# Kernel tuning notes

Measured on AMD Instinct MI355X. Metric: run time of the kernel, lower is better.

Reference implementation:

```python
import jax, jax.numpy as jnp
import numpy as np

B, H, W, D, C = 2, 16, 16, 16, 128
UNITS = 128
BN_EPS = 1e-3  # keras BatchNormalization default epsilon


def setup_inputs() -> dict:
    key = jax.random.key(0)
    ks = jax.random.split(key, 12)
    lim = np.sqrt(3.0 / C)  # VarianceScaling(1.0, fan_avg, uniform)
    inp = {
        "x": jax.random.normal(ks[0], (B, H, W, D, C), dtype=jnp.float32),
        "gamma": jnp.ones((C,), jnp.float32),
        "beta": jnp.zeros((C,), jnp.float32),
        "moving_mean": jax.random.normal(ks[1], (C,), jnp.float32) * 0.1,
        "moving_var": jnp.ones((C,), jnp.float32) + 0.1 * jax.random.uniform(ks[2], (C,)),
        "Wq": jax.random.uniform(ks[3], (C, UNITS), jnp.float32, -lim, lim),
        "bq": jnp.zeros((UNITS,), jnp.float32),
        "Wk": jax.random.uniform(ks[4], (C, UNITS), jnp.float32, -lim, lim),
        "bk": jnp.zeros((UNITS,), jnp.float32),
        "Wv": jax.random.uniform(ks[5], (C, UNITS), jnp.float32, -lim, lim),
        "bv": jnp.zeros((UNITS,), jnp.float32),
        # proj uses kernel_init(0.0) -> effectively ~0; use tiny scale to keep grads nonzero
        "Wp": jax.random.uniform(ks[6], (UNITS, UNITS), jnp.float32, -1e-5, 1e-5),
        "bp": jnp.zeros((UNITS,), jnp.float32),
    }
    return inp


def reference(x, gamma, beta, moving_mean, moving_var, Wq, bq, Wk, bk, Wv, bv, Wp, bp):
    # BatchNormalization (inference mode): per-channel affine normalization
    xn = (x - moving_mean) * jax.lax.rsqrt(moving_var + BN_EPS) * gamma + beta
    b, h, w, d, c = xn.shape
    n = h * w * d
    scale = jnp.asarray(UNITS, jnp.float32) ** -0.5
    q = (xn @ Wq + bq).reshape(b, n, UNITS)
    k = (xn @ Wk + bk).reshape(b, n, UNITS)
    v = (xn @ Wv + bv).reshape(b, n, UNITS)
    # full self-attention over flattened 3D spatial dims: [b, n, n] scores
    attn = jax.nn.softmax(jnp.einsum('bnc,bmc->bnm', q, k) * scale, axis=-1)
    proj = jnp.einsum('bnm,bmc->bnc', attn, v).reshape(b, h, w, d, UNITS)
    proj = proj @ Wp + bp
    return xn + proj
```

## Files before the change

kernel.cpp:

```cpp
#include <hip/hip_runtime.h>
#include <hip/hip_bf16.h>

using bh8     = __attribute__((ext_vector_type(8))) short;
using floatx4 = __attribute__((ext_vector_type(4))) float;

#define MFMA16 __builtin_amdgcn_mfma_f32_16x16x32_bf16

__device__ __forceinline__ float b2f(short s) {
    union { unsigned u; float f; } v; v.u = ((unsigned)(unsigned short)s) << 16; return v.f;
}
__device__ __forceinline__ short f2b(float f) {
    union { float f; unsigned u; } v; v.f = f;
    unsigned r = (v.u + 0x7fffu + ((v.u >> 16) & 1u)) >> 16;
    return (short)r;
}
__device__ __forceinline__ float ldf(const void* p, int i, bool f32) {
    return f32 ? ((const float*)p)[i] : b2f(((const short*)p)[i]);
}
__device__ __forceinline__ bool detect_f32(const void* gamma) {
    return ((*(const unsigned*)gamma) & 0xFFFFu) == 0u;
}
__device__ __forceinline__ void gl2lds16(const short* g, short* l) {
    __builtin_amdgcn_global_load_lds(
        (const __attribute__((address_space(1))) void*)g,
        (__attribute__((address_space(3))) void*)l, 16, 0, 0);
}

#define LDW 136

__global__ __launch_bounds__(256) void k_bn_qkv(
    const void* __restrict__ xp,
    const void* __restrict__ gp, const void* __restrict__ bep,
    const void* __restrict__ mmp, const void* __restrict__ mvp,
    const void* __restrict__ Wqp, const void* __restrict__ bqp,
    const void* __restrict__ Wkp, const void* __restrict__ bkp,
    const void* __restrict__ Wvp, const void* __restrict__ bvp,
    short* __restrict__ Qo, short* __restrict__ Ko, short* __restrict__ Vt)
{
    __shared__ float sS[128], sT[128];
    __shared__ __align__(16) short Wt[128 * LDW];
    const bool f32 = detect_f32(gp);
    const int tid = threadIdx.x, wave = tid >> 6, lane = tid & 63;
    const int lq = lane >> 4, lr = lane & 15;
    const int g = blockIdx.x >> 8;
    const int tile = blockIdx.x & 255;
    const int qrow = tile * 32 + (wave >> 1) * 16;
    const int u0 = (wave & 1) * 64;

    if (tid < 128) {
        float ga = ldf(gp, tid, f32), be = ldf(bep, tid, f32);
        float mm = ldf(mmp, tid, f32), mv = ldf(mvp, tid, f32);
        float s = ga * rsqrtf(mv + 1e-3f);
        sS[tid] = s;
        sT[tid] = be - mm * s;
    }

    const void* W  = (g == 0) ? Wqp : ((g == 1) ? Wkp : Wvp);
    const void* bb = (g == 0) ? bqp : ((g == 1) ? bkp : bvp);

    if (f32) {
        for (int it = 0; it < 16; ++it) {
            int f = (it * 256 + tid) * 4;
            int c = f >> 7, u = f & 127;
            floatx4 wv = *(const floatx4*)((const float*)W + f);
            #pragma unroll
            for (int jj = 0; jj < 4; ++jj) {
                int j = (jj + (tid >> 1)) & 3;
                Wt[(u + j) * LDW + c] = f2b(wv[j]);
            }
        }
    } else {
        for (int it = 0; it < 8; ++it) {
            int f = (it * 256 + tid) * 8;
            int c = f >> 7, u = f & 127;
            bh8 wv = *(const bh8*)((const short*)W + f);
            #pragma unroll
            for (int jj = 0; jj < 8; ++jj) {
                int j = (jj + tid) & 7;
                Wt[(u + j) * LDW + c] = wv[j];
            }
        }
    }
    __syncthreads();

    bh8 a[4];
    #pragma unroll
    for (int ks = 0; ks < 4; ++ks) {
        int c0 = ks * 32 + lq * 8;
        floatx4 s0 = *(const floatx4*)(&sS[c0]), s1 = *(const floatx4*)(&sS[c0 + 4]);
        floatx4 t0 = *(const floatx4*)(&sT[c0]), t1 = *(const floatx4*)(&sT[c0 + 4]);
        bh8 af;
        if (f32) {
            const float* xr = (const float*)xp + (size_t)(qrow + lr) * 128 + c0;
            floatx4 x0 = *(const floatx4*)xr, x1 = *(const floatx4*)(xr + 4);
            #pragma unroll
            for (int j = 0; j < 4; ++j) {
                af[j]     = f2b(x0[j] * s0[j] + t0[j]);
                af[j + 4] = f2b(x1[j] * s1[j] + t1[j]);
            }
        } else {
            bh8 xv = *(const bh8*)((const short*)xp + (size_t)(qrow + lr) * 128 + c0);
            #pragma unroll
            for (int j = 0; j < 4; ++j) {
                af[j]     = f2b(b2f(xv[j]) * s0[j] + t0[j]);
                af[j + 4] = f2b(b2f(xv[j + 4]) * s1[j] + t1[j]);
            }
        }
        a[ks] = af;
    }

    floatx4 acc[4] = {};
    #pragma unroll
    for (int ks = 0; ks < 4; ++ks)
        #pragma unroll
        for (int t = 0; t < 4; ++t) {
            bh8 b = *(const bh8*)(&Wt[(u0 + t * 16 + lr) * LDW + ks * 32 + lq * 8]);
            acc[t] = MFMA16(a[ks], b, acc[t], 0, 0, 0);
        }

    if (g < 2) {
        #pragma unroll
        for (int t = 0; t < 4; ++t) {
            int u = u0 + t * 16 + lr;
            float bias = ldf(bb, u, f32);
            #pragma unroll
            for (int r = 0; r < 4; ++r) {
                int grow = qrow + lq * 4 + r;
                short vb = f2b(acc[t][r] + bias);
                if (g == 0) Qo[(size_t)grow * 128 + u] = vb;
                else        Ko[(size_t)grow * 128 + u] = vb;
            }
        }
    } else {
        __syncthreads();
        short* sVt = Wt;
        #pragma unroll
        for (int t = 0; t < 4; ++t) {
            int u = u0 + t * 16 + lr;
            float bias = ldf(bb, u, f32);
            #pragma unroll
            for (int r = 0; r < 4; ++r) {
                int n = (wave >> 1) * 16 + lq * 4 + r;
                sVt[u * 40 + n] = f2b(acc[t][r] + bias);
            }
        }
        __syncthreads();
        int u = tid >> 1, nh = tid & 1;
        int n0g = tile * 32;
        int bsb = n0g >> 12, nn = (n0g & 4095) + nh * 16;
        bh8 v0 = *(const bh8*)(&sVt[u * 40 + nh * 16]);
        bh8 v1 = *(const bh8*)(&sVt[u * 40 + nh * 16 + 8]);
        short* dst = Vt + (size_t)bsb * 128 * 4096 + (size_t)u * 4096 + nn;
        *(bh8*)dst = v0;
        *(bh8*)(dst + 8) = v1;
    }
}

#define PLDA 40

__global__ __launch_bounds__(128, 2) void k_attn(
    const short* __restrict__ Qg, const short* __restrict__ Kg,
    const short* __restrict__ Vtg, short* __restrict__ Op,
    float* __restrict__ Lq)
{
    __shared__ __align__(16) short sK[2][32 * 128];
    __shared__ __align__(16) short sV[2][128 * 32];
    __shared__ __align__(16) short sP[2][32 * PLDA];

    const int tid = threadIdx.x, wave = tid >> 6, lane = tid & 63;
    const int lq = lane >> 4, lr = lane & 15;
    const int qt = blockIdx.x >> 2, kq = blockIdx.x & 3;
    const int mq = qt * 64, bs = mq >> 12, key0q = kq * 1024;
    const short* Kb = Kg + (size_t)bs * 4096 * 128;
    const short* Vb = Vtg + (size_t)bs * 128 * 4096;
    const int qrow0 = mq + wave * 32;

    bh8 aq[2][4];
    #pragma unroll
    for (int rt = 0; rt < 2; ++rt)
        #pragma unroll
        for (int ks = 0; ks < 4; ++ks)
            aq[rt][ks] = *(const bh8*)(Qg + (size_t)(qrow0 + rt * 16 + lr) * 128 + ks * 32 + lq * 8);

    const int kKey = lane >> 4, kCh = lane & 15;
    const int vU   = lane >> 2, vCh = lane & 3;

    floatx4 accO[2][8] = {};
    float lsum[2][4] = {};
    const float c2 = 0.12751743f;
    const float m2 = 11.541560f;
    short* Pw = &sP[wave][0];

    #pragma unroll
    for (int rd = 0; rd < 4; ++rd) {
        int key = wave * 16 + rd * 4 + kKey;
        gl2lds16(Kb + (size_t)(key0q + key) * 128 + ((kCh ^ (key & 7)) << 3),
                 &sK[0][(wave * 16 + rd * 4) * 128]);
    }
    #pragma unroll
    for (int rd = 0; rd < 4; ++rd) {
        int u = wave * 64 + rd * 16 + vU;
        gl2lds16(Vb + (size_t)u * 4096 + key0q + ((vCh ^ ((u >> 1) & 3)) << 3),
                 &sV[0][(wave * 64 + rd * 16) * 32]);
    }
    __syncthreads();

    for (int it = 0; it < 32; ++it) {
        const int p = it & 1;
        if (it < 31) {
            const int key1 = key0q + (it + 1) * 32;
            #pragma unroll
            for (int rd = 0; rd < 4; ++rd) {
                int key = wave * 16 + rd * 4 + kKey;
                gl2lds16(Kb + (size_t)(key1 + key) * 128 + ((kCh ^ (key & 7)) << 3),
                         &sK[p ^ 1][(wave * 16 + rd * 4) * 128]);
            }
            #pragma unroll
            for (int rd = 0; rd < 4; ++rd) {
                int u = wave * 64 + rd * 16 + vU;
                gl2lds16(Vb + (size_t)u * 4096 + key1 + ((vCh ^ ((u >> 1) & 3)) << 3),
                         &sV[p ^ 1][(wave * 64 + rd * 16) * 32]);
            }
        }

        const short* sKp = &sK[p][0];
        const short* sVp = &sV[p][0];

        floatx4 s[2][2];
        #pragma unroll
        for (int rt = 0; rt < 2; ++rt)
            #pragma unroll
            for (int t = 0; t < 2; ++t)
                s[rt][t] = floatx4{};
        #pragma unroll
        for (int t = 0; t < 2; ++t)
            #pragma unroll
            for (int ks = 0; ks < 4; ++ks) {
                bh8 b = *(const bh8*)(&sKp[(t * 16 + lr) * 128 +
                                           (((ks * 4 + lq) ^ (lr & 7)) << 3)]);
                #pragma unroll
                for (int rt = 0; rt < 2; ++rt)
                    s[rt][t] = MFMA16(aq[rt][ks], b, s[rt][t], 0, 0, 0);
            }

        #pragma unroll
        for (int rt = 0; rt < 2; ++rt)
            #pragma unroll
            for (int t = 0; t < 2; ++t)
                #pragma unroll
                for (int r = 0; r < 4; ++r) {
                    float e = exp2f(fmaf(s[rt][t][r], c2, -m2));
                    s[rt][t][r] = e;
                    lsum[rt][r] += e;
                }

        #pragma unroll
        for (int rt = 0; rt < 2; ++rt)
            #pragma unroll
            for (int t = 0; t < 2; ++t)
                #pragma unroll
                for (int r = 0; r < 4; ++r)
                    Pw[(rt * 16 + lq * 4 + r) * PLDA + t * 16 + lr] = f2b(s[rt][t][r]);

        bh8 ap[2];
        #pragma unroll
        for (int rt = 0; rt < 2; ++rt)
            ap[rt] = *(const bh8*)(&Pw[(rt * 16 + lr) * PLDA + lq * 8]);

        #pragma unroll
        for (int t = 0; t < 8; ++t) {
            int u = t * 16 + lr;
            bh8 b = *(const bh8*)(&sVp[u * 32 + ((lq ^ ((lr >> 1) & 3)) << 3)]);
            #pragma unroll
            for (int rt = 0; rt < 2; ++rt)
                accO[rt][t] = MFMA16(ap[rt], b, accO[rt][t], 0, 0, 0);
        }
        if (it < 31) __syncthreads();
    }

    #pragma unroll
    for (int rt = 0; rt < 2; ++rt)
        #pragma unroll
        for (int r = 0; r < 4; ++r) {
            float v = lsum[rt][r];
            v += __shfl_xor(v, 1, 16);
            v += __shfl_xor(v, 2, 16);
            v += __shfl_xor(v, 4, 16);
            v += __shfl_xor(v, 8, 16);
            lsum[rt][r] = v;
        }
    if (lr == 0) {
        #pragma unroll
        for (int rt = 0; rt < 2; ++rt)
            #pragma unroll
            for (int r = 0; r < 4; ++r)
                Lq[(size_t)kq * 8192 + qrow0 + rt * 16 + lq * 4 + r] = lsum[rt][r];
    }
    short* Ob = Op + (size_t)kq * 8192 * 128;
    #pragma unroll
    for (int rt = 0; rt < 2; ++rt)
        #pragma unroll
        for (int t = 0; t < 8; ++t)
            #pragma unroll
            for (int r = 0; r < 4; ++r)
                Ob[(size_t)(qrow0 + rt * 16 + lq * 4 + r) * 128 + t * 16 + lr]
                    = f2b(accO[rt][t][r]);
}

__global__ __launch_bounds__(256) void k_proj(
    const short* __restrict__ Op, const float* __restrict__ Lq,
    const void* __restrict__ Wpp, const void* __restrict__ bpp,
    const void* __restrict__ xp,
    const void* __restrict__ gp, const void* __restrict__ bep,
    const void* __restrict__ mmp, const void* __restrict__ mvp,
    void* __restrict__ outp)
{
    __shared__ float sS[128], sT[128];
    __shared__ __align__(16) short Wt[64 * LDW];
    __shared__ __align__(16) short sO[32 * LDW];
    const bool f32 = detect_f32(gp);
    const int tid = threadIdx.x, wave = tid >> 6, lane = tid & 63;
    const int lq = lane >> 4, lr = lane & 15;
    const int uh = blockIdx.x & 1;
    const int tile = blockIdx.x >> 1;
    const int row0 = tile * 32;
    const int rh = wave >> 1, us = wave & 1;

    if (tid < 128) {
        float ga = ldf(gp, tid, f32), be = ldf(bep, tid, f32);
        float mm = ldf(mmp, tid, f32), mv = ldf(mvp, tid, f32);
        float s = ga * rsqrtf(mv + 1e-3f);
        sS[tid] = s;
        sT[tid] = be - mm * s;
    }

    if (f32) {
        for (int it = 0; it < 8; ++it) {
            int f = (it * 256 + tid) * 4;
            int c = f >> 6, ul = f & 63;
            floatx4 wv = *(const floatx4*)((const float*)Wpp + (size_t)c * 128 + uh * 64 + ul);
            #pragma unroll
            for (int jj = 0; jj < 4; ++jj) {
                int j = (jj + (tid >> 1)) & 3;
                Wt[(ul + j) * LDW + c] = f2b(wv[j]);
            }
        }
    } else {
        for (int it = 0; it < 4; ++it) {
            int f = (it * 256 + tid) * 8;
            int c = f >> 6, ul = f & 63;
            bh8 wv = *(const bh8*)((const short*)Wpp + (size_t)c * 128 + uh * 64 + ul);
            #pragma unroll
            for (int jj = 0; jj < 8; ++jj) {
                int j = (jj + tid) & 7;
                Wt[(ul + j) * LDW + c] = wv[j];
            }
        }
    }

    #pragma unroll
    for (int e = 0; e < 2; ++e) {
        int f = (e * 256 + tid) * 8;
        int row = f >> 7, c = f & 127;
        int grow = row0 + row;
        float L = Lq[grow] + Lq[8192 + grow] + Lq[16384 + grow] + Lq[24576 + grow];
        float invL = 1.0f / L;
        float sum[8] = {};
        #pragma unroll
        for (int w = 0; w < 4; ++w) {
            bh8 p = *(const bh8*)(Op + (size_t)w * 8192 * 128 + (size_t)grow * 128 + c);
            #pragma unroll
            for (int j = 0; j < 8; ++j) sum[j] += b2f(p[j]);
        }
        bh8 o;
        #pragma unroll
        for (int j = 0; j < 8; ++j) o[j] = f2b(sum[j] * invL);
        *(bh8*)(&sO[row * LDW + c]) = o;
    }
    __syncthreads();

    bh8 a[4];
    #pragma unroll
    for (int ks = 0; ks < 4; ++ks)
        a[ks] = *(const bh8*)(&sO[(rh * 16 + lr) * LDW + ks * 32 + lq * 8]);

    floatx4 acc[2] = {};
    #pragma unroll
    for (int ks = 0; ks < 4; ++ks)
        #pragma unroll
        for (int t = 0; t < 2; ++t) {
            bh8 b = *(const bh8*)(&Wt[(us * 32 + t * 16 + lr) * LDW + ks * 32 + lq * 8]);
            acc[t] = MFMA16(a[ks], b, acc[t], 0, 0, 0);
        }

    #pragma unroll
    for (int t = 0; t < 2; ++t) {
        int u = uh * 64 + us * 32 + t * 16 + lr;
        float bias = ldf(bpp, u, f32);
        float su = sS[u], tu = sT[u];
        #pragma unroll
        for (int r = 0; r < 4; ++r) {
            int grow = row0 + rh * 16 + lq * 4 + r;
            float xnv = ldf(xp, grow * 128 + u, f32) * su + tu;
            float v = acc[t][r] + bias + xnv;
            size_t idx = (size_t)grow * 128 + u;
            if (f32) ((float*)outp)[idx] = v;
            else     ((short*)outp)[idx] = f2b(v);
        }
    }
}

extern "C" void kernel_launch(void* const* d_in, const int* in_sizes, int n_in,
                              void* d_out, int out_size, void* d_ws, size_t ws_size,
                              hipStream_t stream)
{
    const void* x     = d_in[0];
    const void* gamma = d_in[1];
    const void* beta  = d_in[2];
    const void* mmean = d_in[3];
    const void* mvar  = d_in[4];
    const void* Wq    = d_in[5];
    const void* bq    = d_in[6];
    const void* Wk    = d_in[7];
    const void* bk    = d_in[8];
    const void* Wv    = d_in[9];
    const void* bv    = d_in[10];
    const void* Wp    = d_in[11];
    const void* bp    = d_in[12];

    char* ws = (char*)d_ws;
    const size_t MB = 1024u * 1024u;
    short* Q     = (short*)(ws + 0 * MB);
    short* K     = (short*)(ws + 2 * MB);
    short* Vt    = (short*)(ws + 4 * MB);
    short* Opart = (short*)(ws + 6 * MB);
    float* Lsum  = (float*)(ws + 14 * MB);

    k_bn_qkv<<<768, 256, 0, stream>>>(x, gamma, beta, mmean, mvar,
                                      Wq, bq, Wk, bk, Wv, bv, Q, K, Vt);
    k_attn<<<512, 128, 0, stream>>>(Q, K, Vt, Opart, Lsum);
    k_proj<<<512, 256, 0, stream>>>(Opart, Lsum, Wp, bp, x,
                                    gamma, beta, mmean, mvar, d_out);
}
```

Baseline: 156.7 us.

## Enlarge QKV tiles and split attention keys eight ways with 4-wave blocks

```diff
diff --git a/kernel.cpp b/kernel.cpp
--- a/kernel.cpp
+++ b/kernel.cpp
@@ -42,10 +42,9 @@
     const bool f32 = detect_f32(gp);
     const int tid = threadIdx.x, wave = tid >> 6, lane = tid & 63;
     const int lq = lane >> 4, lr = lane & 15;
-    const int g = blockIdx.x >> 8;
-    const int tile = blockIdx.x & 255;
-    const int qrow = tile * 32 + (wave >> 1) * 16;
-    const int u0 = (wave & 1) * 64;
+    const int g = blockIdx.x >> 6;
+    const int tile = blockIdx.x & 63;
+    const int row0 = tile * 128 + wave * 32;
 
     if (tid < 128) {
         float ga = ldf(gp, tid, f32), be = ldf(bep, tid, f32);
@@ -83,94 +82,101 @@
     }
     __syncthreads();
 
-    bh8 a[4];
-    #pragma unroll
-    for (int ks = 0; ks < 4; ++ks) {
-        int c0 = ks * 32 + lq * 8;
-        floatx4 s0 = *(const floatx4*)(&sS[c0]), s1 = *(const floatx4*)(&sS[c0 + 4]);
-        floatx4 t0 = *(const floatx4*)(&sT[c0]), t1 = *(const floatx4*)(&sT[c0 + 4]);
-        bh8 af;
-        if (f32) {
-            const float* xr = (const float*)xp + (size_t)(qrow + lr) * 128 + c0;
-            floatx4 x0 = *(const floatx4*)xr, x1 = *(const floatx4*)(xr + 4);
-            #pragma unroll
-            for (int j = 0; j < 4; ++j) {
-                af[j]     = f2b(x0[j] * s0[j] + t0[j]);
-                af[j + 4] = f2b(x1[j] * s1[j] + t1[j]);
-            }
-        } else {
-            bh8 xv = *(const bh8*)((const short*)xp + (size_t)(qrow + lr) * 128 + c0);
-            #pragma unroll
-            for (int j = 0; j < 4; ++j) {
-                af[j]     = f2b(b2f(xv[j]) * s0[j] + t0[j]);
-                af[j + 4] = f2b(b2f(xv[j + 4]) * s1[j] + t1[j]);
-            }
-        }
-        a[ks] = af;
-    }
-
-    floatx4 acc[4] = {};
+    bh8 a[2][4];
+    #pragma unroll
+    for (int rt = 0; rt < 2; ++rt)
+        #pragma unroll
+        for (int ks = 0; ks < 4; ++ks) {
+            int c0 = ks * 32 + lq * 8;
+            floatx4 s0 = *(const floatx4*)(&sS[c0]), s1 = *(const floatx4*)(&sS[c0 + 4]);
+            floatx4 t0 = *(const floatx4*)(&sT[c0]), t1 = *(const floatx4*)(&sT[c0 + 4]);
+            bh8 af;
+            if (f32) {
+                const float* xr = (const float*)xp + (size_t)(row0 + rt * 16 + lr) * 128 + c0;
+                floatx4 x0 = *(const floatx4*)xr, x1 = *(const floatx4*)(xr + 4);
+                #pragma unroll
+                for (int j = 0; j < 4; ++j) {
+                    af[j]     = f2b(x0[j] * s0[j] + t0[j]);
+                    af[j + 4] = f2b(x1[j] * s1[j] + t1[j]);
+                }
+            } else {
+                bh8 xv = *(const bh8*)((const short*)xp + (size_t)(row0 + rt * 16 + lr) * 128 + c0);
+                #pragma unroll
+                for (int j = 0; j < 4; ++j) {
+                    af[j]     = f2b(b2f(xv[j]) * s0[j] + t0[j]);
+                    af[j + 4] = f2b(b2f(xv[j + 4]) * s1[j] + t1[j]);
+                }
+            }
+            a[rt][ks] = af;
+        }
+
+    floatx4 acc[2][8] = {};
     #pragma unroll
     for (int ks = 0; ks < 4; ++ks)
         #pragma unroll
-        for (int t = 0; t < 4; ++t) {
-            bh8 b = *(const bh8*)(&Wt[(u0 + t * 16 + lr) * LDW + ks * 32 + lq * 8]);
-            acc[t] = MFMA16(a[ks], b, acc[t], 0, 0, 0);
+        for (int t = 0; t < 8; ++t) {
+            bh8 b = *(const bh8*)(&Wt[(t * 16 + lr) * LDW + ks * 32 + lq * 8]);
+            #pragma unroll
+            for (int rt = 0; rt < 2; ++rt)
+                acc[rt][t] = MFMA16(a[rt][ks], b, acc[rt][t], 0, 0, 0);
         }
 
     if (g < 2) {
         #pragma unroll
-        for (int t = 0; t < 4; ++t) {
-            int u = u0 + t * 16 + lr;
+        for (int t = 0; t < 8; ++t) {
+            int u = t * 16 + lr;
             float bias = ldf(bb, u, f32);
             #pragma unroll
-            for (int r = 0; r < 4; ++r) {
-                int grow = qrow + lq * 4 + r;
-                short vb = f2b(acc[t][r] + bias);
-                if (g == 0) Qo[(size_t)grow * 128 + u] = vb;
-                else        Ko[(size_t)grow * 128 + u] = vb;
-            }
+            for (int rt = 0; rt < 2; ++rt)
+                #pragma unroll
+                for (int r = 0; r < 4; ++r) {
+                    int grow = row0 + rt * 16 + lq * 4 + r;
+                    short vb = f2b(acc[rt][t][r] + bias);
+                    if (g == 0) Qo[(size_t)grow * 128 + u] = vb;
+                    else        Ko[(size_t)grow * 128 + u] = vb;
+                }
         }
     } else {
         __syncthreads();
         short* sVt = Wt;
         #pragma unroll
-        for (int t = 0; t < 4; ++t) {
-            int u = u0 + t * 16 + lr;
+        for (int t = 0; t < 8; ++t) {
+            int u = t * 16 + lr;
             float bias = ldf(bb, u, f32);
             #pragma unroll
-            for (int r = 0; r < 4; ++r) {
-                int n = (wave >> 1) * 16 + lq * 4 + r;
-                sVt[u * 40 + n] = f2b(acc[t][r] + bias);
-            }
+            for (int rt = 0; rt < 2; ++rt)
+                #pragma unroll
+                for (int r = 0; r < 4; ++r) {
+                    int n = wave * 32 + rt * 16 + lq * 4 + r;
+                    sVt[u * LDW + n] = f2b(acc[rt][t][r] + bias);
+                }
         }
         __syncthreads();
         int u = tid >> 1, nh = tid & 1;
-        int n0g = tile * 32;
-        int bsb = n0g >> 12, nn = (n0g & 4095) + nh * 16;
-        bh8 v0 = *(const bh8*)(&sVt[u * 40 + nh * 16]);
-        bh8 v1 = *(const bh8*)(&sVt[u * 40 + nh * 16 + 8]);
+        int grow0 = tile * 128 + nh * 64;
+        int bsb = grow0 >> 12, nn = grow0 & 4095;
         short* dst = Vt + (size_t)bsb * 128 * 4096 + (size_t)u * 4096 + nn;
-        *(bh8*)dst = v0;
-        *(bh8*)(dst + 8) = v1;
+        #pragma unroll
+        for (int j = 0; j < 8; ++j)
+            *(bh8*)(dst + j * 8) = *(const bh8*)(&sVt[u * LDW + nh * 64 + j * 8]);
     }
 }
 
 #define PLDA 40
 
-__global__ __launch_bounds__(128, 2) void k_attn(
+__global__ __launch_bounds__(256, 2) void k_attn(
     const short* __restrict__ Qg, const short* __restrict__ Kg,
     const short* __restrict__ Vtg, short* __restrict__ Op,
     float* __restrict__ Lq)
 {
     __shared__ __align__(16) short sK[2][32 * 128];
     __shared__ __align__(16) short sV[2][128 * 32];
-    __shared__ __align__(16) short sP[2][32 * PLDA];
+    __shared__ __align__(16) short sP[4][32 * PLDA];
 
     const int tid = threadIdx.x, wave = tid >> 6, lane = tid & 63;
     const int lq = lane >> 4, lr = lane & 15;
-    const int qt = blockIdx.x >> 2, kq = blockIdx.x & 3;
-    const int mq = qt * 64, bs = mq >> 12, key0q = kq * 1024;
+    const int qt = blockIdx.x >> 3, kq = blockIdx.x & 7;
+    const int mq = qt * 128, bs = mq >> 12, key0q = kq * 512;
     const short* Kb = Kg + (size_t)bs * 4096 * 128;
     const short* Vb = Vtg + (size_t)bs * 128 * 4096;
     const int qrow0 = mq + wave * 32;
@@ -192,34 +198,34 @@
     short* Pw = &sP[wave][0];
 
     #pragma unroll
-    for (int rd = 0; rd < 4; ++rd) {
-        int key = wave * 16 + rd * 4 + kKey;
+    for (int rd = 0; rd < 2; ++rd) {
+        int key = wave * 8 + rd * 4 + kKey;
         gl2lds16(Kb + (size_t)(key0q + key) * 128 + ((kCh ^ (key & 7)) << 3),
-                 &sK[0][(wave * 16 + rd * 4) * 128]);
-    }
-    #pragma unroll
-    for (int rd = 0; rd < 4; ++rd) {
-        int u = wave * 64 + rd * 16 + vU;
+                 &sK[0][(wave * 8 + rd * 4) * 128]);
+    }
+    #pragma unroll
+    for (int rd = 0; rd < 2; ++rd) {
+        int u = wave * 32 + rd * 16 + vU;
         gl2lds16(Vb + (size_t)u * 4096 + key0q + ((vCh ^ ((u >> 1) & 3)) << 3),
-                 &sV[0][(wave * 64 + rd * 16) * 32]);
+                 &sV[0][(wave * 32 + rd * 16) * 32]);
     }
     __syncthreads();
 
-    for (int it = 0; it < 32; ++it) {
+    for (int it = 0; it < 16; ++it) {
         const int p = it & 1;
-        if (it < 31) {
+        if (it < 15) {
             const int key1 = key0q + (it + 1) * 32;
             #pragma unroll
-            for (int rd = 0; rd < 4; ++rd) {
-                int key = wave * 16 + rd * 4 + kKey;
+            for (int rd = 0; rd < 2; ++rd) {
+                int key = wave * 8 + rd * 4 + kKey;
                 gl2lds16(Kb + (size_t)(key1 + key) * 128 + ((kCh ^ (key & 7)) << 3),
-                         &sK[p ^ 1][(wave * 16 + rd * 4) * 128]);
-            }
-            #pragma unroll
-            for (int rd = 0; rd < 4; ++rd) {
-                int u = wave * 64 + rd * 16 + vU;
+                         &sK[p ^ 1][(wave * 8 + rd * 4) * 128]);
+            }
+            #pragma unroll
+            for (int rd = 0; rd < 2; ++rd) {
+                int u = wave * 32 + rd * 16 + vU;
                 gl2lds16(Vb + (size_t)u * 4096 + key1 + ((vCh ^ ((u >> 1) & 3)) << 3),
-                         &sV[p ^ 1][(wave * 64 + rd * 16) * 32]);
+                         &sV[p ^ 1][(wave * 32 + rd * 16) * 32]);
             }
         }
 
@@ -275,7 +281,7 @@
             for (int rt = 0; rt < 2; ++rt)
                 accO[rt][t] = MFMA16(ap[rt], b, accO[rt][t], 0, 0, 0);
         }
-        if (it < 31) __syncthreads();
+        if (it < 15) __syncthreads();
     }
 
     #pragma unroll
@@ -363,11 +369,13 @@
         int f = (e * 256 + tid) * 8;
         int row = f >> 7, c = f & 127;
         int grow = row0 + row;
-        float L = Lq[grow] + Lq[8192 + grow] + Lq[16384 + grow] + Lq[24576 + grow];
+        float L = 0.f;
+        #pragma unroll
+        for (int w = 0; w < 8; ++w) L += Lq[(size_t)w * 8192 + grow];
         float invL = 1.0f / L;
         float sum[8] = {};
         #pragma unroll
-        for (int w = 0; w < 4; ++w) {
+        for (int w = 0; w < 8; ++w) {
             bh8 p = *(const bh8*)(Op + (size_t)w * 8192 * 128 + (size_t)grow * 128 + c);
             #pragma unroll
             for (int j = 0; j < 8; ++j) sum[j] += b2f(p[j]);
@@ -434,11 +442,11 @@
     short* K     = (short*)(ws + 2 * MB);
     short* Vt    = (short*)(ws + 4 * MB);
     short* Opart = (short*)(ws + 6 * MB);
-    float* Lsum  = (float*)(ws + 14 * MB);
-
-    k_bn_qkv<<<768, 256, 0, stream>>>(x, gamma, beta, mmean, mvar,
+    float* Lsum  = (float*)(ws + 22 * MB);
+
+    k_bn_qkv<<<192, 256, 0, stream>>>(x, gamma, beta, mmean, mvar,
                                       Wq, bq, Wk, bk, Wv, bv, Q, K, Vt);
-    k_attn<<<512, 128, 0, stream>>>(Q, K, Vt, Opart, Lsum);
+    k_attn<<<512, 256, 0, stream>>>(Q, K, Vt, Opart, Lsum);
     k_proj<<<512, 256, 0, stream>>>(Opart, Lsum, Wp, bp, x,
                                     gamma, beta, mmean, mvar, d_out);
 }
```

Result: faster. 132.9 us (-15.2%).
